# Optimization experiments

Hardware: AMD Instinct MI355X
Metric: run time of the kernel (lower is better)

Reference implementation:

```python
import jax, jax.numpy as jnp
import numpy as np

NUM_SAMPLES = 64
NEAR = 2.0
FAR = 6.0
B = 262144  # 512x512 rays


def setup_inputs() -> dict:
    key = jax.random.key(0)
    k1, k2 = jax.random.split(key)
    rgb = jax.random.uniform(k1, (B, NUM_SAMPLES, 3), dtype=jnp.float32)
    sigma = jax.random.uniform(k2, (B, NUM_SAMPLES), dtype=jnp.float32)
    return {"rgb": rgb, "sigma": sigma}


def reference(rgb, sigma):
    # rgb: [B, S, 3], sigma: [B, S] (raw model density output)
    b, s = sigma.shape
    t_vals = jnp.linspace(NEAR, FAR, s, dtype=sigma.dtype)  # [S]

    alpha = 1.0 - jnp.exp(-sigma)  # [B, S]
    # exclusive cumulative product of transmittance: T_i = prod_{j<i} (1 - alpha_j + eps)
    trans = jnp.cumprod(
        jnp.concatenate([jnp.ones((b, 1), dtype=alpha.dtype), 1.0 - alpha + 1e-10], axis=1),
        axis=1,
    )[:, :-1]  # [B, S]
    weights = alpha * trans  # [B, S]

    rgb_map = jnp.einsum("bs,bsc->bc", weights, rgb)  # [B, 3]
    depth_map = jnp.einsum("bs,s->b", weights, t_vals)  # [B]
    return rgb_map, depth_map
```

## Files before the change

kernel.cpp:

```cpp
#include <hip/hip_runtime.h>


#define NSAMP 64
#define WAVES_PER_BLOCK 4

__global__ __launch_bounds__(256) void nerf_render_kernel(
    const float* __restrict__ rgb,
    const float* __restrict__ sigma,
    float* __restrict__ rgb_map,
    float* __restrict__ depth_map,
    int n_rays)
{
    const int lane = threadIdx.x & 63;
    const int wave = threadIdx.x >> 6;
    const int ray  = blockIdx.x * WAVES_PER_BLOCK + wave;
    if (ray >= n_rays) return;

    const float sg = sigma[(size_t)ray * NSAMP + lane];
    const float* rp = rgb + ((size_t)ray * NSAMP + lane) * 3;
    const float r = rp[0];
    const float g = rp[1];
    const float b = rp[2];

    const float alpha = 1.0f - expf(-sg);
    const float v = 1.0f - alpha + 1e-10f;

    float p = v;
    #pragma unroll
    for (int d = 1; d < 64; d <<= 1) {
        float o = __shfl_up(p, d, 64);
        if (lane >= d) p *= o;
    }
    float T = __shfl_up(p, 1, 64);
    if (lane == 0) T = 1.0f;

    const float w = alpha * T;
    const float tv = 2.0f + (float)lane * (4.0f / 63.0f);

    float cr = w * r;
    float cg = w * g;
    float cb = w * b;
    float cd = w * tv;

    #pragma unroll
    for (int d = 32; d > 0; d >>= 1) {
        cr += __shfl_down(cr, d, 64);
        cg += __shfl_down(cg, d, 64);
        cb += __shfl_down(cb, d, 64);
        cd += __shfl_down(cd, d, 64);
    }

    if (lane == 0) {
        float* o = rgb_map + (size_t)ray * 3;
        o[0] = cr;
        o[1] = cg;
        o[2] = cb;
        depth_map[ray] = cd;
    }
}

extern "C" void kernel_launch(void* const* d_in, const int* in_sizes, int n_in,
                              void* d_out, int out_size, void* d_ws, size_t ws_size,
                              hipStream_t stream) {
    const float* rgb   = (const float*)d_in[0];
    const float* sigma = (const float*)d_in[1];
    const int n_rays = in_sizes[1] / NSAMP;

    float* rgb_map   = (float*)d_out;
    float* depth_map = (float*)d_out + (size_t)n_rays * 3;

    const int blocks = (n_rays + WAVES_PER_BLOCK - 1) / WAVES_PER_BLOCK;
    nerf_render_kernel<<<blocks, WAVES_PER_BLOCK * 64, 0, stream>>>(
        rgb, sigma, rgb_map, depth_map, n_rays);
}
```

Baseline: 307.2 us.

## Split each ray across four threads with serial scan and vector loads

Assigns 16 samples per thread and 4 threads per ray instead of one wave per ray. Each thread reads its samples with float4 loads, runs a sequential transmittance product and weighted accumulation, then combines segments with a small shuffle prefix and reduction. The intent is to cut shuffle-heavy 64-lane scans and reductions and raise bytes per load instruction. The trade-off is more registers per thread, strided per-thread loads with weaker coalescing across lanes, and a switch to the faster, less precise __expf.

```diff
diff --git a/kernel.cpp b/kernel.cpp
--- a/kernel.cpp
+++ b/kernel.cpp
@@ -2,59 +2,69 @@
 
 
 #define NSAMP 64
-#define WAVES_PER_BLOCK 4
+#define QS 16
+#define TPR 4
 
-__global__ __launch_bounds__(256) void nerf_render_kernel(
+__global__ __launch_bounds__(256, 4) void nerf_render_kernel(
     const float* __restrict__ rgb,
     const float* __restrict__ sigma,
     float* __restrict__ rgb_map,
     float* __restrict__ depth_map,
     int n_rays)
 {
-    const int lane = threadIdx.x & 63;
-    const int wave = threadIdx.x >> 6;
-    const int ray  = blockIdx.x * WAVES_PER_BLOCK + wave;
+    const int tid = blockIdx.x * blockDim.x + threadIdx.x;
+    const int ray = tid >> 2;
+    const int q   = tid & 3;
     if (ray >= n_rays) return;
 
-    const float sg = sigma[(size_t)ray * NSAMP + lane];
-    const float* rp = rgb + ((size_t)ray * NSAMP + lane) * 3;
-    const float r = rp[0];
-    const float g = rp[1];
-    const float b = rp[2];
+    const float4* sg4 = (const float4*)(sigma + (size_t)tid * QS);
+    const float4* rg4 = (const float4*)(rgb + (size_t)tid * (QS * 3));
 
-    const float alpha = 1.0f - expf(-sg);
-    const float v = 1.0f - alpha + 1e-10f;
-
-    float p = v;
+    float sg[QS];
     #pragma unroll
-    for (int d = 1; d < 64; d <<= 1) {
-        float o = __shfl_up(p, d, 64);
-        if (lane >= d) p *= o;
+    for (int k = 0; k < QS / 4; ++k) {
+        float4 v = sg4[k];
+        sg[4*k+0] = v.x; sg[4*k+1] = v.y; sg[4*k+2] = v.z; sg[4*k+3] = v.w;
     }
-    float T = __shfl_up(p, 1, 64);
-    if (lane == 0) T = 1.0f;
-
-    const float w = alpha * T;
-    const float tv = 2.0f + (float)lane * (4.0f / 63.0f);
-
-    float cr = w * r;
-    float cg = w * g;
-    float cb = w * b;
-    float cd = w * tv;
-
+    float rg[QS * 3];
     #pragma unroll
-    for (int d = 32; d > 0; d >>= 1) {
-        cr += __shfl_down(cr, d, 64);
-        cg += __shfl_down(cg, d, 64);
-        cb += __shfl_down(cb, d, 64);
-        cd += __shfl_down(cd, d, 64);
+    for (int k = 0; k < (QS * 3) / 4; ++k) {
+        float4 v = rg4[k];
+        rg[4*k+0] = v.x; rg[4*k+1] = v.y; rg[4*k+2] = v.z; rg[4*k+3] = v.w;
     }
 
-    if (lane == 0) {
-        float* o = rgb_map + (size_t)ray * 3;
-        o[0] = cr;
-        o[1] = cg;
-        o[2] = cb;
+    const float tstep = 4.0f / 63.0f;
+    const float tbase = 2.0f + (float)(q * QS) * tstep;
+    float T = 1.0f;
+    float cr = 0.0f, cg = 0.0f, cb = 0.0f, cd = 0.0f;
+    #pragma unroll
+    for (int j = 0; j < QS; ++j) {
+        float e = __expf(-sg[j]);
+        float a = 1.0f - e;
+        float v = e + 1e-10f;
+        float w = a * T;
+        T *= v;
+        cr = fmaf(w, rg[3*j+0], cr);
+        cg = fmaf(w, rg[3*j+1], cg);
+        cb = fmaf(w, rg[3*j+2], cb);
+        cd = fmaf(w, tbase + (float)j * tstep, cd);
+    }
+
+    float P = T;
+    float o1 = __shfl_up(P, 1, TPR); if (q >= 1) P *= o1;
+    float o2 = __shfl_up(P, 2, TPR); if (q >= 2) P *= o2;
+    float pref = __shfl_up(P, 1, TPR); if (q == 0) pref = 1.0f;
+
+    cr *= pref; cg *= pref; cb *= pref; cd *= pref;
+
+    cr += __shfl_xor(cr, 1); cg += __shfl_xor(cg, 1);
+    cb += __shfl_xor(cb, 1); cd += __shfl_xor(cd, 1);
+    cr += __shfl_xor(cr, 2); cg += __shfl_xor(cg, 2);
+    cb += __shfl_xor(cb, 2); cd += __shfl_xor(cd, 2);
+
+    if (q == 0) {
+        float* out = rgb_map + (size_t)ray * 3;
+        out[0] = cr; out[1] = cg; out[2] = cb;
         depth_map[ray] = cd;
     }
 }
@@ -69,7 +79,9 @@
     float* rgb_map   = (float*)d_out;
     float* depth_map = (float*)d_out + (size_t)n_rays * 3;
 
-    const int blocks = (n_rays + WAVES_PER_BLOCK - 1) / WAVES_PER_BLOCK;
-    nerf_render_kernel<<<blocks, WAVES_PER_BLOCK * 64, 0, stream>>>(
+    const int threads = 256;
+    const int total   = n_rays * TPR;
+    const int blocks  = (total + threads - 1) / threads;
+    nerf_render_kernel<<<blocks, threads, 0, stream>>>(
         rgb, sigma, rgb_map, depth_map, n_rays);
 }
```

After: 320.4 us. +4.3%, slower.
